# Kernel optimization log

Measured on AMD Instinct MI355X. Metric: run time of the kernel, lower is better.

The kernel has to match this reference:

```python
import jax, jax.numpy as jnp
import numpy as np

B = 8192
DIMS = [1024, 1024, 1024, 1024]  # input, hidden0, hidden1, output
RANK = 64


def _apg_layer(x, Wm, bm, U, V, b, activate):
    # hyper-net (MLP_Layer with no hidden units == single Linear): generates rank*rank weights per sample
    w = (x @ Wm.T + bm).reshape(x.shape[0], RANK, RANK)   # [B, r, r]
    u = x @ U.T                                           # U_matrix: [B, r]
    # (u.unsqueeze(-1) * w).sum(-2) == per-sample matvec
    h = jnp.einsum('br,brs->bs', u, w)                    # [B, r]
    out = h @ V.T + b                                     # V_matrix + static bias: [B, out]
    return jax.nn.relu(out) if activate else out


def setup_inputs() -> dict:
    key = jax.random.key(0)
    ks = jax.random.split(key, 16)
    inp = {"x": jax.random.normal(ks[0], (B, DIMS[0]), dtype=jnp.float32)}
    ki = 1
    for l in range(3):
        din, dout = DIMS[l], DIMS[l + 1]
        inp[f"Wm{l}"] = jax.random.normal(ks[ki], (RANK * RANK, din), dtype=jnp.float32) * (1.0 / np.sqrt(din)); ki += 1
        inp[f"bm{l}"] = jnp.zeros((RANK * RANK,), dtype=jnp.float32)
        inp[f"U{l}"] = jax.random.normal(ks[ki], (RANK, din), dtype=jnp.float32) * (1.0 / np.sqrt(din)); ki += 1
        inp[f"V{l}"] = jax.random.normal(ks[ki], (dout, RANK), dtype=jnp.float32) * (1.0 / np.sqrt(RANK)); ki += 1
        inp[f"b{l}"] = jnp.zeros((dout,), dtype=jnp.float32)
    return inp


def reference(x, Wm0, bm0, U0, V0, b0, Wm1, bm1, U1, V1, b1, Wm2, bm2, U2, V2, b2):
    h = _apg_layer(x, Wm0, bm0, U0, V0, b0, activate=True)   # hidden layer 0 + ReLU
    h = _apg_layer(h, Wm1, bm1, U1, V1, b1, activate=True)   # hidden layer 1 + ReLU
    out = _apg_layer(h, Wm2, bm2, U2, V2, b2, activate=False)  # output layer, no activation
    return out
```

## Files before the change

kernel.cpp:

```cpp
#include <hip/hip_runtime.h>
#include <stdint.h>

typedef short bf16x8_t __attribute__((ext_vector_type(8)));
typedef short bf16x4_t __attribute__((ext_vector_type(4)));
typedef float f32x4_t __attribute__((ext_vector_type(4)));
typedef unsigned short u16x4_t __attribute__((ext_vector_type(4)));
typedef unsigned short u16x8_t __attribute__((ext_vector_type(8)));

#define DEV static __device__ __forceinline__

DEV float bf2f(unsigned short u) {
  union { unsigned int i; float f; } v; v.i = ((unsigned int)u) << 16; return v.f;
}
DEV unsigned short f2bf(float f) {
  union { float f; unsigned int i; } v; v.f = f;
  unsigned int x = v.i;
  unsigned int lsb = (x >> 16) & 1u;
  x += 0x7fffu + lsb;
  return (unsigned short)(x >> 16);
}

struct CvtSeg {
  const float* src[3];
  unsigned short* dst[3];
  int bstart[4];
};

DEV void cvt_block(const CvtSeg& cs, int vb, int tid) {
  int seg = (vb >= cs.bstart[1] ? 1 : 0) + (vb >= cs.bstart[2] ? 1 : 0);
  int local = (vb - cs.bstart[seg]) * 256 + tid;
  float4 v = ((const float4*)cs.src[seg])[local];
  u16x4_t o = { f2bf(v.x), f2bf(v.y), f2bf(v.z), f2bf(v.w) };
  *(u16x4_t*)&cs.dst[seg][local * 4] = o;
}

DEV void cvt_block512(const CvtSeg& cs, int vb, int tid) {
  int seg = (vb >= cs.bstart[1] ? 1 : 0) + (vb >= cs.bstart[2] ? 1 : 0);
  int local = (vb - cs.bstart[seg]) * 512 + tid;
  float4 v = ((const float4*)cs.src[seg])[local];
  u16x4_t o = { f2bf(v.x), f2bf(v.y), f2bf(v.z), f2bf(v.w) };
  *(u16x4_t*)&cs.dst[seg][local * 4] = o;
}

__global__ __launch_bounds__(256) void k_cvt(CvtSeg cs) {
  cvt_block(cs, blockIdx.x, threadIdx.x);
}

__global__ __launch_bounds__(256, 2) void xu_fused(
    const float* __restrict__ x,
    const unsigned short* __restrict__ U0,
    unsigned short* __restrict__ xb,
    unsigned short* __restrict__ u_out) {
  __shared__ unsigned short tlds[4 * 16 * 72];
  __shared__ float upart[4 * 16 * 68];

  const int tid = threadIdx.x;
  const int lane = tid & 63;
  const int w = tid >> 6;
  const int fr = lane & 15;
  const int quad = lane >> 4;
  const int rowBase = blockIdx.x * 16;

  unsigned short* tl = &tlds[w * 16 * 72];
  const int m2 = lane >> 2;
  const int kc = (lane & 3) * 16;

  f32x4_t uacc[4];
#pragma unroll
  for (int n = 0; n < 4; n++) uacc[n] = f32x4_t{0.f, 0.f, 0.f, 0.f};

  for (int it = 0; it < 4; ++it) {
    const int cb = w * 256 + it * 64;

    {
      const float* xp = x + (size_t)(rowBase + m2) * 1024 + cb + kc;
      float4 v0 = *(const float4*)(xp);
      float4 v1 = *(const float4*)(xp + 4);
      float4 v2 = *(const float4*)(xp + 8);
      float4 v3 = *(const float4*)(xp + 12);
      u16x8_t o0 = { f2bf(v0.x), f2bf(v0.y), f2bf(v0.z), f2bf(v0.w),
                     f2bf(v1.x), f2bf(v1.y), f2bf(v1.z), f2bf(v1.w) };
      u16x8_t o1 = { f2bf(v2.x), f2bf(v2.y), f2bf(v2.z), f2bf(v2.w),
                     f2bf(v3.x), f2bf(v3.y), f2bf(v3.z), f2bf(v3.w) };
      *(u16x8_t*)&tl[m2 * 72 + kc] = o0;
      *(u16x8_t*)&tl[m2 * 72 + kc + 8] = o1;
      unsigned short* xo = xb + (size_t)(rowBase + m2) * 1024 + cb + kc;
      *(u16x8_t*)xo = o0;
      *(u16x8_t*)(xo + 8) = o1;
    }

#pragma unroll
    for (int ks = 0; ks < 2; ++ks) {
      bf16x8_t at = *(const bf16x8_t*)&tl[fr * 72 + ks * 32 + quad * 8];
#pragma unroll
      for (int n = 0; n < 4; n++) {
        bf16x8_t bu = *(const bf16x8_t*)&U0[(size_t)(n * 16 + fr) * 1024 + cb +
                                            ks * 32 + quad * 8];
        uacc[n] = __builtin_amdgcn_mfma_f32_16x16x32_bf16(at, bu, uacc[n], 0, 0, 0);
      }
    }
  }

  {
    float* up = &upart[w * 16 * 68];
#pragma unroll
    for (int n = 0; n < 4; n++)
#pragma unroll
      for (int r = 0; r < 4; r++)
        up[(quad * 4 + r) * 68 + n * 16 + fr] = uacc[n][r];
  }
  __syncthreads();
  {
    int m = tid >> 4;
    int c0 = (tid & 15) * 4;
    f32x4_t s = {0.f, 0.f, 0.f, 0.f};
#pragma unroll
    for (int wv = 0; wv < 4; wv++)
      s += *(const f32x4_t*)&upart[wv * 16 * 68 + m * 68 + c0];
    u16x4_t o = { f2bf(s[0]), f2bf(s[1]), f2bf(s[2]), f2bf(s[3]) };
    *(u16x4_t*)&u_out[(size_t)(rowBase + m) * 64 + c0] = o;
  }
}

#define GLD(gp, lp)                                              \
  __builtin_amdgcn_global_load_lds(                              \
      (const __attribute__((address_space(1))) void*)(gp),       \
      (__attribute__((address_space(3))) void*)(lp), 16, 0, 0)

__global__ __launch_bounds__(512, 2) void k_hyper(
    const unsigned short* __restrict__ A,
    const unsigned short* __restrict__ Wmb,
    const unsigned short* __restrict__ ug,
    const float* __restrict__ bm,
    unsigned short* __restrict__ h_out,
    CvtSeg cs) {
  __shared__ unsigned short lds[65536];

  if (blockIdx.x >= 512) {
    cvt_block512(cs, blockIdx.x - 512, threadIdx.x);
    return;
  }

  unsigned short* As = lds;
  unsigned short* Bs = lds + 32768;

  const int tid = threadIdx.x;
  const int lane = tid & 63;
  const int w = tid >> 6;
  const int wr = w >> 2;
  const int wc = w & 3;
  const int bx = blockIdx.x & 15;
  const int by = blockIdx.x >> 4;
  const int rowBase = by * 256;
  const int colBase = bx * 256;
  const int fr = lane & 15;
  const int quad = lane >> 4;

  const int lrow = lane >> 2;
  const int lchunk = (lane & 3) ^ (lrow & 3);
  const int tr0 = w * 16 + lrow;
  const int tr1 = 128 + w * 16 + lrow;
  const unsigned short* gA0 = A + (size_t)(rowBase + tr0) * 1024 + lchunk * 8;
  const unsigned short* gA1 = A + (size_t)(rowBase + tr1) * 1024 + lchunk * 8;
  const int ct0 = colBase + tr0;
  const int ct1 = colBase + tr1;
  const unsigned short* gB0 =
      Wmb + (size_t)(((ct0 & 63) << 6) | (ct0 >> 6)) * 1024 + lchunk * 8;
  const unsigned short* gB1 =
      Wmb + (size_t)(((ct1 & 63) << 6) | (ct1 >> 6)) * 1024 + lchunk * 8;
  const int dst0 = w * 512;
  const int dst1 = 4096 + w * 512;

  const int aoff = (wr * 128 + fr) * 32 + ((quad ^ (fr & 3)) * 8);
  const int boff = (wc * 64 + fr) * 32 + ((quad ^ (fr & 3)) * 8);

  f32x4_t acc[8][4];
#pragma unroll
  for (int i = 0; i < 8; i++)
#pragma unroll
    for (int j = 0; j < 4; j++) acc[i][j] = f32x4_t{0.f, 0.f, 0.f, 0.f};

#define STAGE_A(t) do { int sl_ = (t) & 3;                  \
    GLD(gA0 + (t) * 32, &As[sl_ * 8192 + dst0]);            \
    GLD(gA1 + (t) * 32, &As[sl_ * 8192 + dst1]); } while (0)
#define STAGE_B(t) do { int sl_ = (t) & 3;                  \
    GLD(gB0 + (t) * 32, &Bs[sl_ * 8192 + dst0]);            \
    GLD(gB1 + (t) * 32, &Bs[sl_ * 8192 + dst1]); } while (0)

  STAGE_A(0); STAGE_B(0); STAGE_A(1); STAGE_B(1);
  asm volatile("s_waitcnt vmcnt(4)" ::: "memory");
  __builtin_amdgcn_s_barrier();

  for (int t = 0; t < 32; ++t) {
    const unsigned short* Asl = &As[(t & 3) * 8192];
    const unsigned short* Bsl = &Bs[(t & 3) * 8192];
    bf16x8_t a0[4], b[4];
#pragma unroll
    for (int i = 0; i < 4; i++) a0[i] = *(const bf16x8_t*)&Asl[aoff + i * 512];
#pragma unroll
    for (int n = 0; n < 4; n++) b[n] = *(const bf16x8_t*)&Bsl[boff + n * 512];
    if (t < 30) STAGE_A(t + 2);
    __builtin_amdgcn_s_barrier();
    asm volatile("s_waitcnt lgkmcnt(0)" ::: "memory");
    __builtin_amdgcn_s_setprio(1);
#pragma unroll
    for (int i = 0; i < 4; i++)
#pragma unroll
      for (int n = 0; n < 4; n++)
        acc[i][n] =
            __builtin_amdgcn_mfma_f32_16x16x32_bf16(a0[i], b[n], acc[i][n], 0, 0, 0);
    __builtin_amdgcn_s_setprio(0);
    __builtin_amdgcn_s_barrier();
    bf16x8_t a1[4];
#pragma unroll
    for (int i = 0; i < 4; i++)
      a1[i] = *(const bf16x8_t*)&Asl[aoff + (i + 4) * 512];
    if (t < 30) STAGE_B(t + 2);
    __builtin_amdgcn_s_barrier();
    asm volatile("s_waitcnt lgkmcnt(0)" ::: "memory");
    __builtin_amdgcn_s_setprio(1);
#pragma unroll
    for (int i = 0; i < 4; i++)
#pragma unroll
      for (int n = 0; n < 4; n++)
        acc[i + 4][n] = __builtin_amdgcn_mfma_f32_16x16x32_bf16(a1[i], b[n],
                                                                acc[i + 4][n], 0, 0, 0);
    __builtin_amdgcn_s_setprio(0);
    if (t < 30) { asm volatile("s_waitcnt vmcnt(4)" ::: "memory"); }
    else        { asm volatile("s_waitcnt vmcnt(0)" ::: "memory"); }
    __builtin_amdgcn_s_barrier();
  }

  __syncthreads();

  {
    int row = tid >> 1;
    int c0 = (tid & 1) * 32;
    const unsigned short* up = ug + (size_t)(rowBase + row) * 64 + c0;
    bf16x8_t v0 = *(const bf16x8_t*)(up);
    bf16x8_t v1 = *(const bf16x8_t*)(up + 8);
    bf16x8_t v2 = *(const bf16x8_t*)(up + 16);
    bf16x8_t v3 = *(const bf16x8_t*)(up + 24);
#pragma unroll
    for (int m = 0; m < 8; m++) {
      lds[(c0 + m) * 264 + row] = (unsigned short)v0[m];
      lds[(c0 + 8 + m) * 264 + row] = (unsigned short)v1[m];
      lds[(c0 + 16 + m) * 264 + row] = (unsigned short)v2[m];
      lds[(c0 + 24 + m) * 264 + row] = (unsigned short)v3[m];
    }
  }
  __syncthreads();

  const int s = bx * 4 + wc;
  float bmv[4];
#pragma unroll
  for (int j = 0; j < 4; j++) bmv[j] = bm[(j * 16 + fr) * 64 + s];

#pragma unroll
  for (int i = 0; i < 8; i++) {
    int row0 = wr * 128 + i * 16 + quad * 4;
    bf16x4_t uv[4];
#pragma unroll
    for (int j = 0; j < 4; j++)
      uv[j] = *(const bf16x4_t*)&lds[(j * 16 + fr) * 264 + row0];
#pragma unroll
    for (int r = 0; r < 4; r++) {
      float p = 0.f;
#pragma unroll
      for (int j = 0; j < 4; j++)
        p += bf2f((unsigned short)uv[j][r]) * (acc[i][j][r] + bmv[j]);
      p += __shfl_xor(p, 1, 64);
      p += __shfl_xor(p, 2, 64);
      p += __shfl_xor(p, 4, 64);
      p += __shfl_xor(p, 8, 64);
      if (fr == 0)
        h_out[(size_t)(rowBase + row0 + r) * 64 + s] = f2bf(p);
    }
  }
}

__global__ __launch_bounds__(256, 2) void vu_fused(
    const unsigned short* __restrict__ h,
    const unsigned short* __restrict__ Vb,
    const float* __restrict__ bias,
    const unsigned short* __restrict__ Un,
    unsigned short* __restrict__ act,
    unsigned short* __restrict__ u_out) {
  __shared__ unsigned short tlds[4 * 16 * 72];
  __shared__ float upart[4 * 16 * 68];

  const int tid = threadIdx.x;
  const int lane = tid & 63;
  const int w = tid >> 6;
  const int fr = lane & 15;
  const int quad = lane >> 4;
  const int rowBase = blockIdx.x * 16;

  unsigned short* tl = &tlds[w * 16 * 72];

  bf16x8_t ah0 = *(const bf16x8_t*)&h[(size_t)(rowBase + fr) * 64 + quad * 8];
  bf16x8_t ah1 = *(const bf16x8_t*)&h[(size_t)(rowBase + fr) * 64 + 32 + quad * 8];

  f32x4_t uacc[4];
#pragma unroll
  for (int n = 0; n < 4; n++) uacc[n] = f32x4_t{0.f, 0.f, 0.f, 0.f};

  for (int it = 0; it < 4; ++it) {
    const int cb = w * 256 + it * 64;

    f32x4_t tacc[4];
#pragma unroll
    for (int nt = 0; nt < 4; nt++) {
      const unsigned short* vrow = Vb + (size_t)(cb + nt * 16 + fr) * 64;
      bf16x8_t b0 = *(const bf16x8_t*)&vrow[quad * 8];
      bf16x8_t b1 = *(const bf16x8_t*)&vrow[32 + quad * 8];
      f32x4_t z = {0.f, 0.f, 0.f, 0.f};
      z = __builtin_amdgcn_mfma_f32_16x16x32_bf16(ah0, b0, z, 0, 0, 0);
      tacc[nt] = __builtin_amdgcn_mfma_f32_16x16x32_bf16(ah1, b1, z, 0, 0, 0);
    }

#pragma unroll
    for (int nt = 0; nt < 4; nt++) {
      float bv = bias[cb + nt * 16 + fr];
#pragma unroll
      for (int r = 0; r < 4; r++) {
        float v = tacc[nt][r] + bv;
        v = v > 0.f ? v : 0.f;
        tl[(quad * 4 + r) * 72 + nt * 16 + fr] = f2bf(v);
      }
    }

    {
      int m2 = lane >> 2;
      int kc = (lane & 3) * 16;
      bf16x8_t t0 = *(const bf16x8_t*)&tl[m2 * 72 + kc];
      bf16x8_t t1 = *(const bf16x8_t*)&tl[m2 * 72 + kc + 8];
      unsigned short* ap = act + (size_t)(rowBase + m2) * 1024 + cb + kc;
      *(bf16x8_t*)ap = t0;
      *(bf16x8_t*)(ap + 8) = t1;
    }

#pragma unroll
    for (int ks = 0; ks < 2; ++ks) {
      bf16x8_t at = *(const bf16x8_t*)&tl[fr * 72 + ks * 32 + quad * 8];
#pragma unroll
      for (int n = 0; n < 4; n++) {
        bf16x8_t bu = *(const bf16x8_t*)&Un[(size_t)(n * 16 + fr) * 1024 + cb +
                                            ks * 32 + quad * 8];
        uacc[n] = __builtin_amdgcn_mfma_f32_16x16x32_bf16(at, bu, uacc[n], 0, 0, 0);
      }
    }
  }

  {
    float* up = &upart[w * 16 * 68];
#pragma unroll
    for (int n = 0; n < 4; n++)
#pragma unroll
      for (int r = 0; r < 4; r++)
        up[(quad * 4 + r) * 68 + n * 16 + fr] = uacc[n][r];
  }
  __syncthreads();
  {
    int m = tid >> 4;
    int c0 = (tid & 15) * 4;
    f32x4_t s = {0.f, 0.f, 0.f, 0.f};
#pragma unroll
    for (int wv = 0; wv < 4; wv++)
      s += *(const f32x4_t*)&upart[wv * 16 * 68 + m * 68 + c0];
    u16x4_t o = { f2bf(s[0]), f2bf(s[1]), f2bf(s[2]), f2bf(s[3]) };
    *(u16x4_t*)&u_out[(size_t)(rowBase + m) * 64 + c0] = o;
  }
}

__global__ __launch_bounds__(256, 2) void k_final(
    const unsigned short* __restrict__ A, const unsigned short* __restrict__ B,
    const float* __restrict__ bias, float* __restrict__ Cout) {
  __shared__ unsigned short As[128 * 64];
  __shared__ unsigned short Bs[128 * 64];

  const int tid = threadIdx.x;
  const int lane = tid & 63;
  const int w = tid >> 6;
  const int wrow0 = (w & 1) * 64;
  const int wcol0 = (w >> 1) * 64;
  const int rowBase = blockIdx.y * 128;
  const int colBase = blockIdx.x * 128;

  const int rl = lane >> 3;
  const int kbg = (lane & 7) ^ rl;
  const int fr = lane & 15;
  const int quad = lane >> 4;

  f32x4_t acc[4][4];
#pragma unroll
  for (int i = 0; i < 4; i++)
#pragma unroll
    for (int j = 0; j < 4; j++) acc[i][j] = f32x4_t{0.f, 0.f, 0.f, 0.f};

  __syncthreads();
#pragma unroll
  for (int jj = 0; jj < 4; ++jj) {
    int tr = w * 32 + jj * 8 + rl;
    const unsigned short* ga = A + (size_t)(rowBase + tr) * 64 + kbg * 8;
    const unsigned short* gb = B + (size_t)(colBase + tr) * 64 + kbg * 8;
    __builtin_amdgcn_global_load_lds(
        (const __attribute__((address_space(1))) void*)ga,
        (__attribute__((address_space(3))) void*)&As[(w * 32 + jj * 8) * 64],
        16, 0, 0);
    __builtin_amdgcn_global_load_lds(
        (const __attribute__((address_space(1))) void*)gb,
        (__attribute__((address_space(3))) void*)&Bs[(w * 32 + jj * 8) * 64],
        16, 0, 0);
  }
  __syncthreads();

#pragma unroll
  for (int ks = 0; ks < 2; ++ks) {
    bf16x8_t a[4], b[4];
#pragma unroll
    for (int i = 0; i < 4; i++) {
      int m = wrow0 + i * 16 + fr;
      int slot = (ks * 4 + quad) ^ (m & 7);
      a[i] = *(const bf16x8_t*)&As[m * 64 + slot * 8];
    }
#pragma unroll
    for (int j = 0; j < 4; j++) {
      int n = wcol0 + j * 16 + fr;
      int slot = (ks * 4 + quad) ^ (n & 7);
      b[j] = *(const bf16x8_t*)&Bs[n * 64 + slot * 8];
    }
#pragma unroll
    for (int i = 0; i < 4; i++)
#pragma unroll
      for (int j = 0; j < 4; j++)
        acc[i][j] = __builtin_amdgcn_mfma_f32_16x16x32_bf16(a[i], b[j],
                                                            acc[i][j], 0, 0, 0);
  }

#pragma unroll
  for (int j = 0; j < 4; j++) {
    int col = colBase + wcol0 + j * 16 + fr;
    float bv = bias[col];
#pragma unroll
    for (int i = 0; i < 4; i++) {
#pragma unroll
      for (int r = 0; r < 4; r++) {
        int row = rowBase + wrow0 + i * 16 + quad * 4 + r;
        Cout[(size_t)row * 1024 + col] = acc[i][j][r] + bv;
      }
    }
  }
}

extern "C" void kernel_launch(void* const* d_in, const int* in_sizes, int n_in,
                              void* d_out, int out_size, void* d_ws,
                              size_t ws_size, hipStream_t stream) {
  const float* x = (const float*)d_in[0];
  const float* Wm[3] = {(const float*)d_in[1], (const float*)d_in[6], (const float*)d_in[11]};
  const float* bm[3] = {(const float*)d_in[2], (const float*)d_in[7], (const float*)d_in[12]};
  const float* U[3]  = {(const float*)d_in[3], (const float*)d_in[8], (const float*)d_in[13]};
  const float* V[3]  = {(const float*)d_in[4], (const float*)d_in[9], (const float*)d_in[14]};
  const float* bs[3] = {(const float*)d_in[5], (const float*)d_in[10], (const float*)d_in[15]};

  char* p = (char*)d_ws;
  unsigned short* xb = (unsigned short*)p;  p += 8192UL * 1024 * 2;
  unsigned short* act = (unsigned short*)p; p += 8192UL * 1024 * 2;
  unsigned short* Wmb[3];
  for (int l = 0; l < 3; l++) { Wmb[l] = (unsigned short*)p; p += 4096UL * 1024 * 2; }
  unsigned short* Ub[3];
  for (int l = 0; l < 3; l++) { Ub[l] = (unsigned short*)p; p += 64UL * 1024 * 2; }
  unsigned short* Vb[3];
  for (int l = 0; l < 3; l++) { Vb[l] = (unsigned short*)p; p += 1024UL * 64 * 2; }
  unsigned short* hb = (unsigned short*)p;  p += 8192UL * 64 * 2;
  unsigned short* ug = (unsigned short*)p;  p += 8192UL * 64 * 2;

  CvtSeg c0;
  c0.src[0] = Wm[0]; c0.dst[0] = Wmb[0];
  c0.src[1] = U[0];  c0.dst[1] = Ub[0];
  c0.src[2] = U[0];  c0.dst[2] = Ub[0];
  c0.bstart[0] = 0; c0.bstart[1] = 4096; c0.bstart[2] = 4160; c0.bstart[3] = 4160;
  k_cvt<<<4160, 256, 0, stream>>>(c0);

  xu_fused<<<512, 256, 0, stream>>>(x, Ub[0], xb, ug);

  CvtSeg ch[3];
  ch[0].src[0] = Wm[1]; ch[0].dst[0] = Wmb[1];
  ch[0].src[1] = U[1];  ch[0].dst[1] = Ub[1];
  ch[0].src[2] = V[0];  ch[0].dst[2] = Vb[0];
  ch[0].bstart[0] = 0; ch[0].bstart[1] = 2048; ch[0].bstart[2] = 2080; ch[0].bstart[3] = 2112;
  ch[1].src[0] = Wm[2]; ch[1].dst[0] = Wmb[2];
  ch[1].src[1] = U[2];  ch[1].dst[1] = Ub[2];
  ch[1].src[2] = V[1];  ch[1].dst[2] = Vb[1];
  ch[1].bstart[0] = 0; ch[1].bstart[1] = 2048; ch[1].bstart[2] = 2080; ch[1].bstart[3] = 2112;
  ch[2].src[0] = V[2]; ch[2].dst[0] = Vb[2];
  ch[2].src[1] = V[2]; ch[2].dst[1] = Vb[2];
  ch[2].src[2] = V[2]; ch[2].dst[2] = Vb[2];
  ch[2].bstart[0] = 0; ch[2].bstart[1] = 32; ch[2].bstart[2] = 32; ch[2].bstart[3] = 32;

  const int hyperGrid[3] = {512 + 2112, 512 + 2112, 512 + 32};

  const unsigned short* cur = xb;
  for (int l = 0; l < 3; l++) {
    k_hyper<<<hyperGrid[l], 512, 0, stream>>>(cur, Wmb[l], ug, bm[l], hb, ch[l]);
    if (l < 2) {
      vu_fused<<<512, 256, 0, stream>>>(hb, Vb[l], bs[l], Ub[l + 1], act, ug);
      cur = act;
    } else {
      k_final<<<dim3(8, 64), 256, 0, stream>>>(hb, Vb[2], bs[2], (float*)d_out);
    }
  }
}
```

Before: 437.0 us.

## Restructure hyper GEMM mainloop to K=64 double-buffered four-phase pipeline

```diff
diff --git a/kernel.cpp b/kernel.cpp
--- a/kernel.cpp
+++ b/kernel.cpp
@@ -127,7 +127,7 @@
       (const __attribute__((address_space(1))) void*)(gp),       \
       (__attribute__((address_space(3))) void*)(lp), 16, 0, 0)
 
-__global__ __launch_bounds__(512, 2) void k_hyper(
+__global__ __launch_bounds__(512, 1) void k_hyper(
     const unsigned short* __restrict__ A,
     const unsigned short* __restrict__ Wmb,
     const unsigned short* __restrict__ ug,
@@ -156,23 +156,41 @@
   const int fr = lane & 15;
   const int quad = lane >> 4;
 
-  const int lrow = lane >> 2;
-  const int lchunk = (lane & 3) ^ (lrow & 3);
-  const int tr0 = w * 16 + lrow;
-  const int tr1 = 128 + w * 16 + lrow;
-  const unsigned short* gA0 = A + (size_t)(rowBase + tr0) * 1024 + lchunk * 8;
-  const unsigned short* gA1 = A + (size_t)(rowBase + tr1) * 1024 + lchunk * 8;
-  const int ct0 = colBase + tr0;
-  const int ct1 = colBase + tr1;
-  const unsigned short* gB0 =
-      Wmb + (size_t)(((ct0 & 63) << 6) | (ct0 >> 6)) * 1024 + lchunk * 8;
-  const unsigned short* gB1 =
-      Wmb + (size_t)(((ct1 & 63) << 6) | (ct1 >> 6)) * 1024 + lchunk * 8;
-  const int dst0 = w * 512;
-  const int dst1 = 4096 + w * 512;
-
-  const int aoff = (wr * 128 + fr) * 32 + ((quad ^ (fr & 3)) * 8);
-  const int boff = (wc * 64 + fr) * 32 + ((quad ^ (fr & 3)) * 8);
+  const int rl = lane >> 3;
+  const int kbg = (lane & 7) ^ rl;
+  const unsigned short* gA[4];
+  const unsigned short* gB[4];
+  int ldst[4];
+#pragma unroll
+  for (int h = 0; h < 2; h++)
+#pragma unroll
+    for (int jj = 0; jj < 2; jj++) {
+      int tr = h * 128 + w * 16 + jj * 8 + rl;
+      gA[h * 2 + jj] = A + (size_t)(rowBase + tr) * 1024 + kbg * 8;
+      int ct = colBase + tr;
+      gB[h * 2 + jj] =
+          Wmb + (size_t)(((ct & 63) << 6) | (ct >> 6)) * 1024 + kbg * 8;
+      ldst[h * 2 + jj] = (h * 128 + w * 16 + jj * 8) * 64;
+    }
+
+#define STAGE_A(t, h) do {                                           \
+    GLD(gA[(h) * 2 + 0] + (t) * 64,                                  \
+        &As[((t) & 1) * 16384 + ldst[(h) * 2 + 0]]);                 \
+    GLD(gA[(h) * 2 + 1] + (t) * 64,                                  \
+        &As[((t) & 1) * 16384 + ldst[(h) * 2 + 1]]); } while (0)
+#define STAGE_B(t, h) do {                                           \
+    GLD(gB[(h) * 2 + 0] + (t) * 64,                                  \
+        &Bs[((t) & 1) * 16384 + ldst[(h) * 2 + 0]]);                 \
+    GLD(gB[(h) * 2 + 1] + (t) * 64,                                  \
+        &Bs[((t) & 1) * 16384 + ldst[(h) * 2 + 1]]); } while (0)
+
+  const int xors = fr & 7;
+  const int aBase = (wr * 128 + fr) * 64;
+  const int a0s = aBase + ((0 + quad) ^ xors) * 8;
+  const int a1s = aBase + ((4 + quad) ^ xors) * 8;
+  const int bBase = (wc * 64 + fr) * 64;
+  const int b0s = bBase + ((0 + quad) ^ xors) * 8;
+  const int b1s = bBase + ((4 + quad) ^ xors) * 8;
 
   f32x4_t acc[8][4];
 #pragma unroll
@@ -180,54 +198,93 @@
 #pragma unroll
     for (int j = 0; j < 4; j++) acc[i][j] = f32x4_t{0.f, 0.f, 0.f, 0.f};
 
-#define STAGE_A(t) do { int sl_ = (t) & 3;                  \
-    GLD(gA0 + (t) * 32, &As[sl_ * 8192 + dst0]);            \
-    GLD(gA1 + (t) * 32, &As[sl_ * 8192 + dst1]); } while (0)
-#define STAGE_B(t) do { int sl_ = (t) & 3;                  \
-    GLD(gB0 + (t) * 32, &Bs[sl_ * 8192 + dst0]);            \
-    GLD(gB1 + (t) * 32, &Bs[sl_ * 8192 + dst1]); } while (0)
-
-  STAGE_A(0); STAGE_B(0); STAGE_A(1); STAGE_B(1);
+  STAGE_A(0, 0); STAGE_A(0, 1); STAGE_B(0, 0); STAGE_B(0, 1);
+  STAGE_A(1, 0); STAGE_A(1, 1);
   asm volatile("s_waitcnt vmcnt(4)" ::: "memory");
   __builtin_amdgcn_s_barrier();
 
-  for (int t = 0; t < 32; ++t) {
-    const unsigned short* Asl = &As[(t & 3) * 8192];
-    const unsigned short* Bsl = &Bs[(t & 3) * 8192];
-    bf16x8_t a0[4], b[4];
-#pragma unroll
-    for (int i = 0; i < 4; i++) a0[i] = *(const bf16x8_t*)&Asl[aoff + i * 512];
-#pragma unroll
-    for (int n = 0; n < 4; n++) b[n] = *(const bf16x8_t*)&Bsl[boff + n * 512];
-    if (t < 30) STAGE_A(t + 2);
+#pragma unroll 2
+  for (int t = 0; t < 16; ++t) {
+    const int d = (t & 1) * 16384;
+    bf16x8_t a[8][2], b[4][2];
+#pragma unroll
+    for (int i = 0; i < 4; i++) {
+      a[i][0] = *(const bf16x8_t*)&As[d + a0s + i * 1024];
+      a[i][1] = *(const bf16x8_t*)&As[d + a1s + i * 1024];
+    }
+#pragma unroll
+    for (int j = 0; j < 2; j++) {
+      b[j][0] = *(const bf16x8_t*)&Bs[d + b0s + j * 1024];
+      b[j][1] = *(const bf16x8_t*)&Bs[d + b1s + j * 1024];
+    }
+    if (t < 15) STAGE_B(t + 1, 0);
+    __builtin_amdgcn_s_setprio(1);
+#pragma unroll
+    for (int i = 0; i < 4; i++)
+#pragma unroll
+      for (int j = 0; j < 2; j++) {
+        acc[i][j] = __builtin_amdgcn_mfma_f32_16x16x32_bf16(a[i][0], b[j][0],
+                                                            acc[i][j], 0, 0, 0);
+        acc[i][j] = __builtin_amdgcn_mfma_f32_16x16x32_bf16(a[i][1], b[j][1],
+                                                            acc[i][j], 0, 0, 0);
+      }
+    __builtin_amdgcn_s_setprio(0);
+    asm volatile("" ::: "memory");
     __builtin_amdgcn_s_barrier();
+#pragma unroll
+    for (int i = 4; i < 8; i++) {
+      a[i][0] = *(const bf16x8_t*)&As[d + a0s + i * 1024];
+      a[i][1] = *(const bf16x8_t*)&As[d + a1s + i * 1024];
+    }
+#pragma unroll
+    for (int j = 2; j < 4; j++) {
+      b[j][0] = *(const bf16x8_t*)&Bs[d + b0s + j * 1024];
+      b[j][1] = *(const bf16x8_t*)&Bs[d + b1s + j * 1024];
+    }
+    if (t < 15) STAGE_B(t + 1, 1);
+    __builtin_amdgcn_s_setprio(1);
+#pragma unroll
+    for (int i = 4; i < 8; i++)
+#pragma unroll
+      for (int j = 0; j < 2; j++) {
+        acc[i][j] = __builtin_amdgcn_mfma_f32_16x16x32_bf16(a[i][0], b[j][0],
+                                                            acc[i][j], 0, 0, 0);
+        acc[i][j] = __builtin_amdgcn_mfma_f32_16x16x32_bf16(a[i][1], b[j][1],
+                                                            acc[i][j], 0, 0, 0);
+      }
+    __builtin_amdgcn_s_setprio(0);
     asm volatile("s_waitcnt lgkmcnt(0)" ::: "memory");
+    __builtin_amdgcn_s_barrier();
+    if (t < 14) STAGE_A(t + 2, 0);
     __builtin_amdgcn_s_setprio(1);
 #pragma unroll
     for (int i = 0; i < 4; i++)
 #pragma unroll
-      for (int n = 0; n < 4; n++)
-        acc[i][n] =
-            __builtin_amdgcn_mfma_f32_16x16x32_bf16(a0[i], b[n], acc[i][n], 0, 0, 0);
+      for (int j = 2; j < 4; j++) {
+        acc[i][j] = __builtin_amdgcn_mfma_f32_16x16x32_bf16(a[i][0], b[j][0],
+                                                            acc[i][j], 0, 0, 0);
+        acc[i][j] = __builtin_amdgcn_mfma_f32_16x16x32_bf16(a[i][1], b[j][1],
+                                                            acc[i][j], 0, 0, 0);
+      }
     __builtin_amdgcn_s_setprio(0);
     __builtin_amdgcn_s_barrier();
-    bf16x8_t a1[4];
-#pragma unroll
-    for (int i = 0; i < 4; i++)
-      a1[i] = *(const bf16x8_t*)&Asl[aoff + (i + 4) * 512];
-    if (t < 30) STAGE_B(t + 2);
-    __builtin_amdgcn_s_barrier();
-    asm volatile("s_waitcnt lgkmcnt(0)" ::: "memory");
+    if (t < 14) STAGE_A(t + 2, 1);
     __builtin_amdgcn_s_setprio(1);
 #pragma unroll
-    for (int i = 0; i < 4; i++)
-#pragma unroll
-      for (int n = 0; n < 4; n++)
-        acc[i + 4][n] = __builtin_amdgcn_mfma_f32_16x16x32_bf16(a1[i], b[n],
-                                                                acc[i + 4][n], 0, 0, 0);
+    for (int i = 4; i < 8; i++)
+#pragma unroll
+      for (int j = 2; j < 4; j++) {
+        acc[i][j] = __builtin_amdgcn_mfma_f32_16x16x32_bf16(a[i][0], b[j][0],
+                                                            acc[i][j], 0, 0, 0);
+        acc[i][j] = __builtin_amdgcn_mfma_f32_16x16x32_bf16(a[i][1], b[j][1],
+                                                            acc[i][j], 0, 0, 0);
+      }
     __builtin_amdgcn_s_setprio(0);
-    if (t < 30) { asm volatile("s_waitcnt vmcnt(4)" ::: "memory"); }
-    else        { asm volatile("s_waitcnt vmcnt(0)" ::: "memory"); }
+    if (t < 14) {
+      asm volatile("s_waitcnt vmcnt(4)" ::: "memory");
+    } else if (t == 14) {
+      asm volatile("s_waitcnt vmcnt(0)" ::: "memory");
+    }
     __builtin_amdgcn_s_barrier();
   }
 
```

After: 482.4 us. 10.4% more time.

## Restructure hyper GEMM mainloop to double-buffered BK=64 tiles with full-tile MFMA phases

Applied to the files above, without the earlier changes.

```diff
diff --git a/kernel.cpp b/kernel.cpp
--- a/kernel.cpp
+++ b/kernel.cpp
@@ -127,7 +127,7 @@
       (const __attribute__((address_space(1))) void*)(gp),       \
       (__attribute__((address_space(3))) void*)(lp), 16, 0, 0)
 
-__global__ __launch_bounds__(512, 2) void k_hyper(
+__global__ __launch_bounds__(512, 1) void k_hyper(
     const unsigned short* __restrict__ A,
     const unsigned short* __restrict__ Wmb,
     const unsigned short* __restrict__ ug,
@@ -156,23 +156,38 @@
   const int fr = lane & 15;
   const int quad = lane >> 4;
 
-  const int lrow = lane >> 2;
-  const int lchunk = (lane & 3) ^ (lrow & 3);
-  const int tr0 = w * 16 + lrow;
-  const int tr1 = 128 + w * 16 + lrow;
-  const unsigned short* gA0 = A + (size_t)(rowBase + tr0) * 1024 + lchunk * 8;
-  const unsigned short* gA1 = A + (size_t)(rowBase + tr1) * 1024 + lchunk * 8;
-  const int ct0 = colBase + tr0;
-  const int ct1 = colBase + tr1;
-  const unsigned short* gB0 =
-      Wmb + (size_t)(((ct0 & 63) << 6) | (ct0 >> 6)) * 1024 + lchunk * 8;
-  const unsigned short* gB1 =
-      Wmb + (size_t)(((ct1 & 63) << 6) | (ct1 >> 6)) * 1024 + lchunk * 8;
-  const int dst0 = w * 512;
-  const int dst1 = 4096 + w * 512;
-
-  const int aoff = (wr * 128 + fr) * 32 + ((quad ^ (fr & 3)) * 8);
-  const int boff = (wc * 64 + fr) * 32 + ((quad ^ (fr & 3)) * 8);
+  const int rl = lane >> 3;
+  const int kbg = (lane & 7) ^ rl;
+  const unsigned short* gA[4];
+  const unsigned short* gB[4];
+  int ldst[4];
+#pragma unroll
+  for (int h = 0; h < 2; h++)
+#pragma unroll
+    for (int jj = 0; jj < 2; jj++) {
+      int tr = h * 128 + w * 16 + jj * 8 + rl;
+      gA[h * 2 + jj] = A + (size_t)(rowBase + tr) * 1024 + kbg * 8;
+      int ct = colBase + tr;
+      gB[h * 2 + jj] =
+          Wmb + (size_t)(((ct & 63) << 6) | (ct >> 6)) * 1024 + kbg * 8;
+      ldst[h * 2 + jj] = (h * 128 + w * 16 + jj * 8) * 64;
+    }
+
+#define STAGE_ALL(t) do { const int db_ = ((t) & 1) * 16384;         \
+    GLD(gA[0] + (t) * 64, &As[db_ + ldst[0]]);                       \
+    GLD(gA[1] + (t) * 64, &As[db_ + ldst[1]]);                       \
+    GLD(gA[2] + (t) * 64, &As[db_ + ldst[2]]);                       \
+    GLD(gA[3] + (t) * 64, &As[db_ + ldst[3]]);                       \
+    GLD(gB[0] + (t) * 64, &Bs[db_ + ldst[0]]);                       \
+    GLD(gB[1] + (t) * 64, &Bs[db_ + ldst[1]]);                       \
+    GLD(gB[2] + (t) * 64, &Bs[db_ + ldst[2]]);                       \
+    GLD(gB[3] + (t) * 64, &Bs[db_ + ldst[3]]); } while (0)
+
+  const int xors = fr & 7;
+  const int aRow = (wr * 128 + fr) * 64;
+  const int bRow = (wc * 64 + fr) * 64;
+  const int slot0 = ((0 + quad) ^ xors) * 8;
+  const int slot1 = ((4 + quad) ^ xors) * 8;
 
   f32x4_t acc[8][4];
 #pragma unroll
@@ -180,54 +195,51 @@
 #pragma unroll
     for (int j = 0; j < 4; j++) acc[i][j] = f32x4_t{0.f, 0.f, 0.f, 0.f};
 
-#define STAGE_A(t) do { int sl_ = (t) & 3;                  \
-    GLD(gA0 + (t) * 32, &As[sl_ * 8192 + dst0]);            \
-    GLD(gA1 + (t) * 32, &As[sl_ * 8192 + dst1]); } while (0)
-#define STAGE_B(t) do { int sl_ = (t) & 3;                  \
-    GLD(gB0 + (t) * 32, &Bs[sl_ * 8192 + dst0]);            \
-    GLD(gB1 + (t) * 32, &Bs[sl_ * 8192 + dst1]); } while (0)
-
-  STAGE_A(0); STAGE_B(0); STAGE_A(1); STAGE_B(1);
-  asm volatile("s_waitcnt vmcnt(4)" ::: "memory");
+  STAGE_ALL(0);
+  asm volatile("s_waitcnt vmcnt(0)" ::: "memory");
   __builtin_amdgcn_s_barrier();
 
-  for (int t = 0; t < 32; ++t) {
-    const unsigned short* Asl = &As[(t & 3) * 8192];
-    const unsigned short* Bsl = &Bs[(t & 3) * 8192];
-    bf16x8_t a0[4], b[4];
-#pragma unroll
-    for (int i = 0; i < 4; i++) a0[i] = *(const bf16x8_t*)&Asl[aoff + i * 512];
-#pragma unroll
-    for (int n = 0; n < 4; n++) b[n] = *(const bf16x8_t*)&Bsl[boff + n * 512];
-    if (t < 30) STAGE_A(t + 2);
+#pragma unroll 2
+  for (int t = 0; t < 16; ++t) {
+    const int d = (t & 1) * 16384;
+    bf16x8_t a[8], b[4];
+#pragma unroll
+    for (int i = 0; i < 8; i++)
+      a[i] = *(const bf16x8_t*)&As[d + aRow + i * 1024 + slot0];
+#pragma unroll
+    for (int j = 0; j < 4; j++)
+      b[j] = *(const bf16x8_t*)&Bs[d + bRow + j * 1024 + slot0];
+    if (t < 15) STAGE_ALL(t + 1);
     __builtin_amdgcn_s_barrier();
     asm volatile("s_waitcnt lgkmcnt(0)" ::: "memory");
+    __builtin_amdgcn_sched_barrier(0);
     __builtin_amdgcn_s_setprio(1);
 #pragma unroll
-    for (int i = 0; i < 4; i++)
-#pragma unroll
-      for (int n = 0; n < 4; n++)
-        acc[i][n] =
-            __builtin_amdgcn_mfma_f32_16x16x32_bf16(a0[i], b[n], acc[i][n], 0, 0, 0);
+    for (int i = 0; i < 8; i++)
+#pragma unroll
+      for (int j = 0; j < 4; j++)
+        acc[i][j] = __builtin_amdgcn_mfma_f32_16x16x32_bf16(a[i], b[j],
+                                                            acc[i][j], 0, 0, 0);
     __builtin_amdgcn_s_setprio(0);
     __builtin_amdgcn_s_barrier();
-    bf16x8_t a1[4];
-#pragma unroll
-    for (int i = 0; i < 4; i++)
-      a1[i] = *(const bf16x8_t*)&Asl[aoff + (i + 4) * 512];
-    if (t < 30) STAGE_B(t + 2);
+#pragma unroll
+    for (int i = 0; i < 8; i++)
+      a[i] = *(const bf16x8_t*)&As[d + aRow + i * 1024 + slot1];
+#pragma unroll
+    for (int j = 0; j < 4; j++)
+      b[j] = *(const bf16x8_t*)&Bs[d + bRow + j * 1024 + slot1];
     __builtin_amdgcn_s_barrier();
     asm volatile("s_waitcnt lgkmcnt(0)" ::: "memory");
+    __builtin_amdgcn_sched_barrier(0);
     __builtin_amdgcn_s_setprio(1);
 #pragma unroll
-    for (int i = 0; i < 4; i++)
-#pragma unroll
-      for (int n = 0; n < 4; n++)
-        acc[i + 4][n] = __builtin_amdgcn_mfma_f32_16x16x32_bf16(a1[i], b[n],
-                                                                acc[i + 4][n], 0, 0, 0);
+    for (int i = 0; i < 8; i++)
+#pragma unroll
+      for (int j = 0; j < 4; j++)
+        acc[i][j] = __builtin_amdgcn_mfma_f32_16x16x32_bf16(a[i], b[j],
+                                                            acc[i][j], 0, 0, 0);
     __builtin_amdgcn_s_setprio(0);
-    if (t < 30) { asm volatile("s_waitcnt vmcnt(4)" ::: "memory"); }
-    else        { asm volatile("s_waitcnt vmcnt(0)" ::: "memory"); }
+    asm volatile("s_waitcnt vmcnt(0)" ::: "memory");
     __builtin_amdgcn_s_barrier();
   }
 
```

Result: faster. 426.7 us (-2.3%).

## Merge split K-step phases into one stage with new LDS swizzle

Applied to the files above, without the earlier changes.

```diff
diff --git a/kernel.cpp b/kernel.cpp
--- a/kernel.cpp
+++ b/kernel.cpp
@@ -127,7 +127,7 @@
       (const __attribute__((address_space(1))) void*)(gp),       \
       (__attribute__((address_space(3))) void*)(lp), 16, 0, 0)
 
-__global__ __launch_bounds__(512, 2) void k_hyper(
+__global__ __launch_bounds__(512, 1) void k_hyper(
     const unsigned short* __restrict__ A,
     const unsigned short* __restrict__ Wmb,
     const unsigned short* __restrict__ ug,
@@ -156,23 +156,29 @@
   const int fr = lane & 15;
   const int quad = lane >> 4;
 
-  const int lrow = lane >> 2;
-  const int lchunk = (lane & 3) ^ (lrow & 3);
-  const int tr0 = w * 16 + lrow;
-  const int tr1 = 128 + w * 16 + lrow;
-  const unsigned short* gA0 = A + (size_t)(rowBase + tr0) * 1024 + lchunk * 8;
-  const unsigned short* gA1 = A + (size_t)(rowBase + tr1) * 1024 + lchunk * 8;
-  const int ct0 = colBase + tr0;
-  const int ct1 = colBase + tr1;
+  const int lr = lane >> 2;
+  const int c = (lane & 3) ^ ((lane >> 3) & 3);
+  const unsigned short* gA0 =
+      A + (size_t)(rowBase + w * 16 + lr) * 1024 + c * 8;
+  const unsigned short* gA1 = gA0 + (size_t)128 * 1024;
+  const int ct0 = colBase + w * 16 + lr;
+  const int ct1 = ct0 + 128;
   const unsigned short* gB0 =
-      Wmb + (size_t)(((ct0 & 63) << 6) | (ct0 >> 6)) * 1024 + lchunk * 8;
+      Wmb + (size_t)(((ct0 & 63) << 6) | (ct0 >> 6)) * 1024 + c * 8;
   const unsigned short* gB1 =
-      Wmb + (size_t)(((ct1 & 63) << 6) | (ct1 >> 6)) * 1024 + lchunk * 8;
-  const int dst0 = w * 512;
-  const int dst1 = 4096 + w * 512;
-
-  const int aoff = (wr * 128 + fr) * 32 + ((quad ^ (fr & 3)) * 8);
-  const int boff = (wc * 64 + fr) * 32 + ((quad ^ (fr & 3)) * 8);
+      Wmb + (size_t)(((ct1 & 63) << 6) | (ct1 >> 6)) * 1024 + c * 8;
+  const int dA0 = w * 512;
+  const int dA1 = 4096 + w * 512;
+
+#define STAGE(t) do { const int sb_ = ((t) & 3) * 8192;              \
+    GLD(gA0 + (t) * 32, &As[sb_ + dA0]);                             \
+    GLD(gA1 + (t) * 32, &As[sb_ + dA1]);                             \
+    GLD(gB0 + (t) * 32, &Bs[sb_ + dA0]);                             \
+    GLD(gB1 + (t) * 32, &Bs[sb_ + dA1]); } while (0)
+
+  const int sl = (quad ^ ((fr >> 1) & 3)) * 8;
+  const int aBase = (wr * 128 + fr) * 32 + sl;
+  const int bBase = (wc * 64 + fr) * 32 + sl;
 
   f32x4_t acc[8][4];
 #pragma unroll
@@ -180,54 +186,34 @@
 #pragma unroll
     for (int j = 0; j < 4; j++) acc[i][j] = f32x4_t{0.f, 0.f, 0.f, 0.f};
 
-#define STAGE_A(t) do { int sl_ = (t) & 3;                  \
-    GLD(gA0 + (t) * 32, &As[sl_ * 8192 + dst0]);            \
-    GLD(gA1 + (t) * 32, &As[sl_ * 8192 + dst1]); } while (0)
-#define STAGE_B(t) do { int sl_ = (t) & 3;                  \
-    GLD(gB0 + (t) * 32, &Bs[sl_ * 8192 + dst0]);            \
-    GLD(gB1 + (t) * 32, &Bs[sl_ * 8192 + dst1]); } while (0)
-
-  STAGE_A(0); STAGE_B(0); STAGE_A(1); STAGE_B(1);
+  STAGE(0); STAGE(1);
   asm volatile("s_waitcnt vmcnt(4)" ::: "memory");
   __builtin_amdgcn_s_barrier();
 
+#pragma unroll 4
   for (int t = 0; t < 32; ++t) {
-    const unsigned short* Asl = &As[(t & 3) * 8192];
-    const unsigned short* Bsl = &Bs[(t & 3) * 8192];
-    bf16x8_t a0[4], b[4];
-#pragma unroll
-    for (int i = 0; i < 4; i++) a0[i] = *(const bf16x8_t*)&Asl[aoff + i * 512];
-#pragma unroll
-    for (int n = 0; n < 4; n++) b[n] = *(const bf16x8_t*)&Bsl[boff + n * 512];
-    if (t < 30) STAGE_A(t + 2);
+    const int d = (t & 3) * 8192;
+    bf16x8_t a[8], b[4];
+#pragma unroll
+    for (int i = 0; i < 8; i++)
+      a[i] = *(const bf16x8_t*)&As[d + aBase + i * 512];
+#pragma unroll
+    for (int j = 0; j < 4; j++)
+      b[j] = *(const bf16x8_t*)&Bs[d + bBase + j * 512];
+    if (t < 30) STAGE(t + 2);
     __builtin_amdgcn_s_barrier();
     asm volatile("s_waitcnt lgkmcnt(0)" ::: "memory");
+    __builtin_amdgcn_sched_barrier(0);
     __builtin_amdgcn_s_setprio(1);
 #pragma unroll
-    for (int i = 0; i < 4; i++)
-#pragma unroll
-      for (int n = 0; n < 4; n++)
-        acc[i][n] =
-            __builtin_amdgcn_mfma_f32_16x16x32_bf16(a0[i], b[n], acc[i][n], 0, 0, 0);
-    __builtin_amdgcn_s_setprio(0);
-    __builtin_amdgcn_s_barrier();
-    bf16x8_t a1[4];
-#pragma unroll
-    for (int i = 0; i < 4; i++)
-      a1[i] = *(const bf16x8_t*)&Asl[aoff + (i + 4) * 512];
-    if (t < 30) STAGE_B(t + 2);
-    __builtin_amdgcn_s_barrier();
-    asm volatile("s_waitcnt lgkmcnt(0)" ::: "memory");
-    __builtin_amdgcn_s_setprio(1);
-#pragma unroll
-    for (int i = 0; i < 4; i++)
-#pragma unroll
-      for (int n = 0; n < 4; n++)
-        acc[i + 4][n] = __builtin_amdgcn_mfma_f32_16x16x32_bf16(a1[i], b[n],
-                                                                acc[i + 4][n], 0, 0, 0);
+    for (int i = 0; i < 8; i++)
+#pragma unroll
+      for (int j = 0; j < 4; j++)
+        acc[i][j] = __builtin_amdgcn_mfma_f32_16x16x32_bf16(a[i], b[j],
+                                                            acc[i][j], 0, 0, 0);
     __builtin_amdgcn_s_setprio(0);
     if (t < 30) { asm volatile("s_waitcnt vmcnt(4)" ::: "memory"); }
-    else        { asm volatile("s_waitcnt vmcnt(0)" ::: "memory"); }
+    else if (t == 30) { asm volatile("s_waitcnt vmcnt(0)" ::: "memory"); }
     __builtin_amdgcn_s_barrier();
   }
 
```

Measured after the change: 433.5 us. About the same (-0.8%).
